# Kernel tuning notes

Hardware: AMD Instinct MI355X
Metric: run time of the kernel (lower is better)

Reference implementation:

```python
import jax, jax.numpy as jnp
import numpy as np

B, L, M = 4, 16384, 256
HID, FDIM, INNER, ODIM = 512, 128, 128, 3
HEADS, DH = 2, 64
NFREQ = 16  # feature_dim // (2 * input_dim)
ALPHA = 10.0
SIGMA_Q = 128.0
SIGMA_LS = (128.0, 32.0, 8.0)


def setup_inputs() -> dict:
    key = jax.random.key(0)
    ks = jax.random.split(key, 16)
    s = 0.02
    nl = len(SIGMA_LS)
    return {
        "x": jax.random.uniform(ks[0], (B, L, 4), jnp.float32),
        "tokens": jax.random.normal(ks[1], (B, M, HID), jnp.float32),
        "w_query": jax.random.normal(ks[2], (FDIM, HID), jnp.float32) * s,
        "b_query": jnp.zeros((HID,), jnp.float32),
        "w_to_q": jax.random.normal(ks[3], (HID, INNER), jnp.float32) * s,
        "w_to_kv": jax.random.normal(ks[4], (HID, 2 * INNER), jnp.float32) * s,
        "w_to_out": jax.random.normal(ks[5], (INNER, HID), jnp.float32) * s,
        "b_to_out": jnp.zeros((HID,), jnp.float32),
        "w_band": jax.random.normal(ks[6], (nl, FDIM, HID), jnp.float32) * s,
        "b_band": jnp.zeros((nl, HID), jnp.float32),
        "w_mod": jax.random.normal(ks[7], (nl, HID, HID), jnp.float32) * s,
        "b_mod": jnp.zeros((nl, HID), jnp.float32),
        "w_hv": jax.random.normal(ks[8], (nl - 1, HID, HID), jnp.float32) * s,
        "b_hv": jnp.zeros((nl - 1, HID), jnp.float32),
        "w_out": jax.random.normal(ks[9], (nl, HID, ODIM), jnp.float32) * s,
        "b_out": jnp.zeros((nl, ODIM), jnp.float32),
        "Dd": 8, "Hh": 16, "Ww": 16, "Tt": 8,
    }


def _calc_gamma(grid, omegas):
    # grid: [L, 4]; omegas: [NFREQ] -> gamma: [L, 4*2*NFREQ] = [L, FDIM]
    arg = jnp.pi * grid[:, :, None] * omegas[None, None, :]
    return jnp.concatenate([jnp.sin(arg), jnp.cos(arg)], axis=-1).reshape(grid.shape[0], -1)


def reference(x, tokens, w_query, b_query, w_to_q, w_to_kv, w_to_out, b_to_out,
              w_band, b_band, w_mod, b_mod, w_hv, b_hv, w_out, b_out, Dd, Hh, Ww, Tt):
    Bn, Ln, _ = x.shape
    m = tokens.shape[1]
    grid = x[0]  # grid shared across batch, exactly as in the torch module (uses x[0])

    # relative-position bias (ALiBi-like) from approximate patch indices
    z_i = (grid[:, 0] * Dd).astype(jnp.int32)
    y_i = (grid[:, 1] * Hh).astype(jnp.int32)
    x_i = (grid[:, 2] * Ww).astype(jnp.int32)
    t_i = (grid[:, 3] * Tt).astype(jnp.int32)
    idx = ((t_i * Dd + z_i) * Hh + y_i) * Ww + x_i  # [L]
    n_tot = Dd * Hh * Ww * Tt
    t = idx.astype(jnp.float32) / n_tot
    tok_pos = (jnp.arange(m, dtype=jnp.float32) + 0.5) / m
    bias = -ALPHA * (t[:, None] - tok_pos[None, :]) ** 2  # [L, m]

    # Fourier-feature query path (shared across batch)
    omegas_q = jnp.logspace(1.0, np.log10(SIGMA_Q), NFREQ, dtype=jnp.float32)
    x_q = jax.nn.relu(_calc_gamma(grid, omegas_q) @ w_query + b_query)  # [L, HID]

    # cross attention with additive bias
    q = (x_q @ w_to_q).reshape(Ln, HEADS, DH).transpose(1, 0, 2)  # [H, L, Dh]
    kv = tokens @ w_to_kv  # [B, m, 2*INNER]
    k, v = jnp.split(kv, 2, axis=-1)
    k = k.reshape(Bn, m, HEADS, DH).transpose(0, 2, 1, 3)  # [B, H, m, Dh]
    v = v.reshape(Bn, m, HEADS, DH).transpose(0, 2, 1, 3)
    sim = jnp.einsum('hld,bhmd->bhlm', q, k) * (DH ** -0.5) + bias[None, None]
    attn = jax.nn.softmax(sim, axis=-1)
    out = jnp.einsum('bhlm,bhmd->bhld', attn, v)
    out = out.transpose(0, 2, 1, 3).reshape(Bn, Ln, HEADS * DH)
    modv = out @ w_to_out + b_to_out  # [B, L, HID]

    # modulated MLP chain with residual hv accumulation
    total = jnp.zeros((Bn, Ln, w_out.shape[-1]), dtype=x.dtype)
    hv = None
    for kk in range(len(SIGMA_LS)):
        omg = jnp.logspace(1.0, np.log10(SIGMA_LS[kk]), NFREQ, dtype=jnp.float32)
        h_l = jax.nn.relu(_calc_gamma(grid, omg) @ w_band[kk] + b_band[kk])  # [L, HID]
        m_l = jax.nn.relu(h_l[None] + modv @ w_mod[kk] + b_mod[kk])  # [B, L, HID]
        if kk == 0:
            hv = m_l
        else:
            hv = jax.nn.relu((m_l + hv) @ w_hv[kk - 1] + b_hv[kk - 1])
        total = total + hv @ w_out[kk] + b_out[kk]
    return total  # [B, L, ODIM]
```

## Files before the change

### kernel.cpp

```cpp
#include <hip/hip_runtime.h>

#define L_N   16384
#define B_N   4
#define M_N   256
#define HID_N 512
#define PI_F  3.14159265358979323846f

typedef short short8 __attribute__((ext_vector_type(8)));
typedef float f32x4 __attribute__((ext_vector_type(4)));

__device__ __forceinline__ ushort f2bf(float f) {
  uint u = __float_as_uint(f);
  uint r = u + 0x7FFF + ((u >> 16) & 1);
  return (ushort)(r >> 16);
}
__device__ __forceinline__ float bf2f(ushort s) {
  return __uint_as_float(((uint)s) << 16);
}
__device__ __forceinline__ void gld_lds16(const void* g, void* s) {
  __builtin_amdgcn_global_load_lds((const __attribute__((address_space(1))) void*)g,
                                   (__attribute__((address_space(3))) void*)s, 16, 0, 0);
}

__global__ __launch_bounds__(256) void k_wt_all(
    const float* __restrict__ w_query, const float* __restrict__ w_to_q,
    const float* __restrict__ w_to_kv, const float* __restrict__ w_to_out,
    const float* __restrict__ w_band, const float* __restrict__ w_mod,
    const float* __restrict__ w_hv,
    ushort* __restrict__ wq_t, ushort* __restrict__ wtq_t,
    ushort* __restrict__ wkv_t, ushort* __restrict__ wto_t,
    ushort* __restrict__ wb_t, ushort* __restrict__ wm_t, ushort* __restrict__ whv_t) {
  __shared__ float t[32][33];
  int tb = blockIdx.x;
  const float* in; ushort* out; int R, C;
  if (tb < 64)        { in = w_query;  out = wq_t;  R = 128; C = 512; }
  else if (tb < 128)  { tb -= 64;  in = w_to_q;   out = wtq_t; R = 512; C = 128; }
  else if (tb < 256)  { tb -= 128; in = w_to_kv;  out = wkv_t; R = 512; C = 256; }
  else if (tb < 320)  { tb -= 256; in = w_to_out; out = wto_t; R = 128; C = 512; }
  else if (tb < 512)  { tb -= 320; int kk = tb >> 6; tb &= 63;
                        in = w_band + (size_t)kk * 65536; out = wb_t + (size_t)kk * 65536; R = 128; C = 512; }
  else if (tb < 1280) { tb -= 512; int kk = tb >> 8; tb &= 255;
                        in = w_mod + (size_t)kk * 262144; out = wm_t + (size_t)kk * 262144; R = 512; C = 512; }
  else                { tb -= 1280; int kk = tb >> 8; tb &= 255;
                        in = w_hv + (size_t)kk * 262144; out = whv_t + (size_t)kk * 262144; R = 512; C = 512; }
  int nbx = C >> 5;
  int bx = (tb % nbx) * 32, by = (tb / nbx) * 32;
  int tx = threadIdx.x & 31, ty = threadIdx.x >> 5;
#pragma unroll
  for (int j = 0; j < 32; j += 8) t[ty + j][tx] = in[(size_t)(by + ty + j) * C + bx + tx];
  __syncthreads();
#pragma unroll
  for (int j = 0; j < 32; j += 8)
    out[(size_t)(bx + ty + j) * R + by + tx] = f2bf(t[tx][ty + j]);
}

__global__ __launch_bounds__(256) void k_cvt(const float* __restrict__ in,
                                             ushort* __restrict__ out, int n4) {
  int i = blockIdx.x * 256 + threadIdx.x;
  if (i >= n4) return;
  float4 v = *(const float4*)&in[(size_t)i * 4];
  ushort* o = &out[(size_t)i * 4];
  o[0] = f2bf(v.x); o[1] = f2bf(v.y); o[2] = f2bf(v.z); o[3] = f2bf(v.w);
}

__global__ __launch_bounds__(256) void k_gamma(const float* __restrict__ x,
                                               ushort* __restrict__ gout) {
  __shared__ float om[16];
  const float lgs[4] = {2.1072099696478683f, 2.1072099696478683f,
                        1.5051499783199058f, 0.9030899869919435f};
  int spec = blockIdx.y;
  float lg = lgs[spec];
  int tid = threadIdx.x;
  if (tid < 16) om[tid] = powf(10.0f, 1.0f + (float)tid * ((lg - 1.0f) * (1.0f / 15.0f)));
  __syncthreads();
  int l0 = blockIdx.x * 16;
  int idx0 = tid * 8;
  int row = idx0 >> 7, f0 = idx0 & 127;
  int c = f0 >> 5;
  float g = x[(size_t)(l0 + row) * 4 + c];
  float base = PI_F * g;
  int w0 = f0 & 31;
  bool is_cos = (w0 >= 16);
  short8 o;
#pragma unroll
  for (int j = 0; j < 8; ++j) {
    int jf = (w0 + j) & 15;
    float arg = base * om[jf];
    float v = is_cos ? __cosf(arg) : __sinf(arg);
    o[j] = (short)f2bf(v);
  }
  *(short8*)&gout[(size_t)spec * L_N * 128 + (size_t)(l0 + row) * 128 + f0] = o;
}

__global__ __launch_bounds__(256) void k_tpos(const float* __restrict__ x,
                                              const int* dD, const int* dH,
                                              const int* dW, const int* dT,
                                              float* __restrict__ tbuf) {
  int l = blockIdx.x * 256 + threadIdx.x;
  float g0 = x[(size_t)l * 4 + 0], g1 = x[(size_t)l * 4 + 1];
  float g2 = x[(size_t)l * 4 + 2], g3 = x[(size_t)l * 4 + 3];
  int Dd = dD[0], Hh = dH[0], Ww = dW[0], Tt = dT[0];
  int zi = (int)(g0 * (float)Dd), yi = (int)(g1 * (float)Hh);
  int xi = (int)(g2 * (float)Ww), ti = (int)(g3 * (float)Tt);
  int idx = ((ti * Dd + zi) * Hh + yi) * Ww + xi;
  tbuf[l] = (float)idx / (float)(Dd * Hh * Ww * Tt);
}

__global__ __launch_bounds__(256, 4) void k_gemm2(
    const ushort* __restrict__ A, long long sA,
    const ushort* __restrict__ Wt,
    const float* __restrict__ bias,
    const ushort* __restrict__ add1,
    const ushort* add2, long long sAdd2,
    ushort* C, long long sC,
    const float* __restrict__ wout,
    float* __restrict__ opb,
    int zoff,
    int N, int K, int do_relu,
    int nbx, int nby, int nz) {
  __shared__ __align__(16) ushort S[128 * 64 * 2];
  __shared__ float woutL[384];
  ushort* As = S;
  ushort* Ws = S + 128 * 64;
  int tid = threadIdx.x;
  int lane = tid & 63, wid = tid >> 6;

  int nwg = nbx * nby * nz;
  int gid0 = blockIdx.x;
  int q = nwg >> 3, r = nwg & 7;
  int xcd = gid0 & 7, rank = gid0 >> 3;
  int sid = (xcd < r) ? (xcd * (q + 1) + rank) : (r * (q + 1) + (xcd - r) * q + rank);
  int z = sid / (nbx * nby);
  int rem = sid - z * (nbx * nby);
  int n0 = (rem % nbx) * 128, r0 = (rem / nbx) * 128;

  A += (size_t)z * sA;
  C += (size_t)z * sC;
  const ushort* a2p = add2 ? add2 + (size_t)z * sAdd2 : nullptr;
  int wr = wid >> 1, wc = wid & 1;
  int ksm = K >> 6;

  f32x4 acc[4][4];
#pragma unroll
  for (int i = 0; i < 4; ++i)
#pragma unroll
    for (int j = 0; j < 4; ++j) acc[i][j] = (f32x4)0.0f;

  for (int t = 0; t < ksm; ++t) {
#pragma unroll
    for (int j = 0; j < 4; ++j) {
      int sig = j * 256 + wid * 64 + lane;
      int rr = sig >> 3, ph = sig & 7, sl = ph ^ (rr & 7);
      gld_lds16(&A[(size_t)(r0 + rr) * K + t * 64 + sl * 8], &As[(size_t)(j * 256 + wid * 64) * 8]);
      gld_lds16(&Wt[(size_t)(n0 + rr) * K + t * 64 + sl * 8], &Ws[(size_t)(j * 256 + wid * 64) * 8]);
    }
    __syncthreads();
#pragma unroll
    for (int ks = 0; ks < 2; ++ks) {
      short8 af[4], bg[4];
#pragma unroll
      for (int fm = 0; fm < 4; ++fm) {
        int row = wr * 64 + fm * 16 + (lane & 15);
        af[fm] = *(const short8*)&As[row * 64 + (((ks * 4 + (lane >> 4)) ^ (row & 7)) * 8)];
      }
#pragma unroll
      for (int fn = 0; fn < 4; ++fn) {
        int nl = wc * 64 + fn * 16 + (lane & 15);
        bg[fn] = *(const short8*)&Ws[nl * 64 + (((ks * 4 + (lane >> 4)) ^ (nl & 7)) * 8)];
      }
#pragma unroll
      for (int fm = 0; fm < 4; ++fm)
#pragma unroll
        for (int fn = 0; fn < 4; ++fn)
          acc[fm][fn] = __builtin_amdgcn_mfma_f32_16x16x32_bf16(af[fm], bg[fn], acc[fm][fn], 0, 0, 0);
    }
    __syncthreads();
  }

  if (wout && tid < 128) {
    woutL[tid * 3 + 0] = wout[(size_t)(n0 + tid) * 3 + 0];
    woutL[tid * 3 + 1] = wout[(size_t)(n0 + tid) * 3 + 1];
    woutL[tid * 3 + 2] = wout[(size_t)(n0 + tid) * 3 + 2];
  }

  float* Ls = (float*)S;
  int row = tid >> 3;
  int c0 = (tid & 7) * 16;
#pragma unroll
  for (int fm = 0; fm < 4; ++fm) {
    if (fm) __syncthreads();
#pragma unroll
    for (int fn = 0; fn < 4; ++fn)
#pragma unroll
      for (int reg = 0; reg < 4; ++reg) {
        int lr = wr * 16 + (lane >> 4) * 4 + reg;
        int lc = wc * 64 + fn * 16 + (lane & 15);
        Ls[lr * 132 + lc] = acc[fm][fn][reg];
      }
    __syncthreads();
    int gr = r0 + (row >> 4) * 64 + fm * 16 + (row & 15);
    float so0 = 0.0f, so1 = 0.0f, so2 = 0.0f;
#pragma unroll
    for (int hh = 0; hh < 2; ++hh) {
      int cc = c0 + hh * 8;
      float v[8];
#pragma unroll
      for (int j = 0; j < 8; ++j) v[j] = Ls[row * 132 + cc + j];
      if (bias) {
#pragma unroll
        for (int j = 0; j < 8; ++j) v[j] += bias[n0 + cc + j];
      }
      if (add1) {
        short8 a1 = *(const short8*)&add1[(size_t)gr * N + n0 + cc];
#pragma unroll
        for (int j = 0; j < 8; ++j) v[j] += bf2f((ushort)a1[j]);
      }
      if (do_relu) {
#pragma unroll
        for (int j = 0; j < 8; ++j) v[j] = fmaxf(v[j], 0.0f);
      }
      if (a2p) {
        short8 a2 = *(const short8*)&a2p[(size_t)gr * N + n0 + cc];
#pragma unroll
        for (int j = 0; j < 8; ++j) v[j] += bf2f((ushort)a2[j]);
      }
      if (wout) {
#pragma unroll
        for (int j = 0; j < 8; ++j) {
          so0 = fmaf(v[j], woutL[(cc + j) * 3 + 0], so0);
          so1 = fmaf(v[j], woutL[(cc + j) * 3 + 1], so1);
          so2 = fmaf(v[j], woutL[(cc + j) * 3 + 2], so2);
        }
      }
      short8 ov;
#pragma unroll
      for (int j = 0; j < 8; ++j) ov[j] = (short)f2bf(v[j]);
      *(short8*)&C[(size_t)gr * N + n0 + cc] = ov;
    }
    if (wout) {
      so0 += __shfl_down(so0, 4); so1 += __shfl_down(so1, 4); so2 += __shfl_down(so2, 4);
      so0 += __shfl_down(so0, 2); so1 += __shfl_down(so1, 2); so2 += __shfl_down(so2, 2);
      so0 += __shfl_down(so0, 1); so1 += __shfl_down(so1, 1); so2 += __shfl_down(so2, 1);
      if ((tid & 7) == 0) {
        int bx = n0 >> 7;
        size_t oi = (((size_t)bx * 4 + (zoff + z)) * L_N + gr) * 3;
        opb[oi + 0] = so0; opb[oi + 1] = so1; opb[oi + 2] = so2;
      }
    }
  }
}

__global__ __launch_bounds__(256) void k_outred(const float* __restrict__ opb,
                                                const float* __restrict__ b_out,
                                                float* __restrict__ out) {
  int i = blockIdx.x * 256 + threadIdx.x;
  if (i >= B_N * L_N) return;
  float a0 = b_out[0] + b_out[3] + b_out[6];
  float a1 = b_out[1] + b_out[4] + b_out[7];
  float a2 = b_out[2] + b_out[5] + b_out[8];
  const size_t SS = (size_t)4 * B_N * L_N * 3;
#pragma unroll
  for (int slot = 0; slot < 3; ++slot)
#pragma unroll
    for (int bx = 0; bx < 4; ++bx) {
      const float* p = opb + slot * SS + (((size_t)bx * B_N * L_N) + i) * 3;
      a0 += p[0]; a1 += p[1]; a2 += p[2];
    }
  out[(size_t)i * 3 + 0] = a0;
  out[(size_t)i * 3 + 1] = a1;
  out[(size_t)i * 3 + 2] = a2;
}

__global__ __launch_bounds__(256) void k_rearr(const ushort* __restrict__ kvtmp,
                                               ushort* __restrict__ kbuf,
                                               ushort* __restrict__ vtb) {
  int i = blockIdx.x * 256 + threadIdx.x;
  int col = i & 255, row = i >> 8;
  int b = row >> 8, m = row & 255;
  ushort v = kvtmp[i];
  if (col < 128)
    kbuf[((size_t)b * 256 + m) * 128 + col] = v;
  else
    vtb[(size_t)b * 128 * 256 + (size_t)(col - 128) * 256 + m] = v;
}

__global__ __launch_bounds__(256) void k_attn_m(const ushort* __restrict__ qbuf,
                                                const float* __restrict__ tbuf,
                                                const ushort* __restrict__ kbuf,
                                                const ushort* __restrict__ vtb,
                                                ushort* __restrict__ attn) {
  __shared__ __align__(16) ushort Kt[256 * 64];
  __shared__ __align__(16) ushort Vt[64 * 256];
  __shared__ __align__(16) ushort Qs[64 * 64];
  __shared__ __align__(16) ushort Pw[4][16 * 40];
  __shared__ float ts[64];
  int tid = threadIdx.x;
  int lane = tid & 63, wid = tid >> 6;
  int l0 = blockIdx.x * 64;
  int h = blockIdx.y;
  int z = blockIdx.z;
  const ushort* kbuf_b = kbuf + (size_t)z * M_N * 128;
  const ushort* vtb_b = vtb + (size_t)z * 128 * M_N;
  ushort* attn_b = attn + (size_t)z * L_N * 128;
#pragma unroll
  for (int j = 0; j < 8; ++j) {
    int sig = j * 256 + wid * 64 + lane;
    int m = sig >> 3, ph = sig & 7, sl = ph ^ (m & 7);
    gld_lds16(&kbuf_b[(size_t)m * 128 + h * 64 + sl * 8], &Kt[(size_t)(j * 256 + wid * 64) * 8]);
  }
#pragma unroll
  for (int j = 0; j < 8; ++j) {
    int sig = j * 256 + wid * 64 + lane;
    int d = sig >> 5, ph = sig & 31, sl = ph ^ ((d & 7) << 2);
    gld_lds16(&vtb_b[(size_t)(h * 64 + d) * 256 + sl * 8], &Vt[(size_t)(j * 256 + wid * 64) * 8]);
  }
#pragma unroll
  for (int j = 0; j < 2; ++j) {
    int sig = j * 256 + wid * 64 + lane;
    int q = sig >> 3, ph = sig & 7, sl = ph ^ (q & 7);
    gld_lds16(&qbuf[(size_t)(l0 + q) * 128 + h * 64 + sl * 8], &Qs[(size_t)(j * 256 + wid * 64) * 8]);
  }
  if (tid < 64) ts[tid] = tbuf[l0 + tid];
  __syncthreads();

  f32x4 s_acc[16];
#pragma unroll
  for (int fn = 0; fn < 16; ++fn) s_acc[fn] = (f32x4)0.0f;
#pragma unroll
  for (int ks = 0; ks < 2; ++ks) {
    int qrow = wid * 16 + (lane & 15);
    short8 aq = *(const short8*)&Qs[qrow * 64 + (((ks * 4 + (lane >> 4)) ^ (qrow & 7)) * 8)];
#pragma unroll
    for (int fn = 0; fn < 16; ++fn) {
      int m = fn * 16 + (lane & 15);
      short8 bk = *(const short8*)&Kt[m * 64 + (((ks * 4 + (lane >> 4)) ^ (m & 7)) * 8)];
      s_acc[fn] = __builtin_amdgcn_mfma_f32_16x16x32_bf16(aq, bk, s_acc[fn], 0, 0, 0);
    }
  }
  float mx[4] = {-1e30f, -1e30f, -1e30f, -1e30f};
#pragma unroll
  for (int fn = 0; fn < 16; ++fn) {
#pragma unroll
    for (int reg = 0; reg < 4; ++reg) {
      int ql = wid * 16 + (lane >> 4) * 4 + reg;
      int m = fn * 16 + (lane & 15);
      float mp = ((float)m + 0.5f) * (1.0f / 256.0f);
      float d = ts[ql] - mp;
      float v = s_acc[fn][reg] * 0.125f - 10.0f * d * d;
      s_acc[fn][reg] = v;
      mx[reg] = fmaxf(mx[reg], v);
    }
  }
#pragma unroll
  for (int reg = 0; reg < 4; ++reg) {
    mx[reg] = fmaxf(mx[reg], __shfl_xor(mx[reg], 1));
    mx[reg] = fmaxf(mx[reg], __shfl_xor(mx[reg], 2));
    mx[reg] = fmaxf(mx[reg], __shfl_xor(mx[reg], 4));
    mx[reg] = fmaxf(mx[reg], __shfl_xor(mx[reg], 8));
  }
  float sm[4] = {0.0f, 0.0f, 0.0f, 0.0f};
#pragma unroll
  for (int fn = 0; fn < 16; ++fn) {
#pragma unroll
    for (int reg = 0; reg < 4; ++reg) {
      float e = __expf(s_acc[fn][reg] - mx[reg]);
      s_acc[fn][reg] = e;
      sm[reg] += e;
    }
  }
#pragma unroll
  for (int reg = 0; reg < 4; ++reg) {
    sm[reg] += __shfl_xor(sm[reg], 1);
    sm[reg] += __shfl_xor(sm[reg], 2);
    sm[reg] += __shfl_xor(sm[reg], 4);
    sm[reg] += __shfl_xor(sm[reg], 8);
  }
  float inv[4];
#pragma unroll
  for (int reg = 0; reg < 4; ++reg) inv[reg] = 1.0f / sm[reg];

  f32x4 o_acc[4];
#pragma unroll
  for (int fn = 0; fn < 4; ++fn) o_acc[fn] = (f32x4)0.0f;
  for (int kk = 0; kk < 8; ++kk) {
#pragma unroll
    for (int fp = 0; fp < 2; ++fp) {
      int fn = kk * 2 + fp;
#pragma unroll
      for (int reg = 0; reg < 4; ++reg) {
        int ql16 = (lane >> 4) * 4 + reg;
        int mc = fp * 16 + (lane & 15);
        Pw[wid][ql16 * 40 + mc] = f2bf(s_acc[fn][reg] * inv[reg]);
      }
    }
    asm volatile("s_waitcnt lgkmcnt(0)" ::: "memory");
    __builtin_amdgcn_sched_barrier(0);
    short8 pa = *(const short8*)&Pw[wid][(lane & 15) * 40 + (lane >> 4) * 8];
#pragma unroll
    for (int fn = 0; fn < 4; ++fn) {
      int dr = fn * 16 + (lane & 15);
      short8 vb = *(const short8*)&Vt[dr * 256 + (((kk * 4 + (lane >> 4)) ^ ((dr & 7) << 2)) * 8)];
      o_acc[fn] = __builtin_amdgcn_mfma_f32_16x16x32_bf16(pa, vb, o_acc[fn], 0, 0, 0);
    }
    asm volatile("s_waitcnt lgkmcnt(0)" ::: "memory");
    __builtin_amdgcn_sched_barrier(0);
  }
#pragma unroll
  for (int fn = 0; fn < 4; ++fn)
#pragma unroll
    for (int reg = 0; reg < 4; ++reg) {
      int ql = l0 + wid * 16 + (lane >> 4) * 4 + reg;
      attn_b[(size_t)ql * 128 + h * 64 + fn * 16 + (lane & 15)] = f2bf(o_acc[fn][reg]);
    }
}

extern "C" void kernel_launch(void* const* d_in, const int* in_sizes, int n_in,
                              void* d_out, int out_size, void* d_ws, size_t ws_size,
                              hipStream_t stream) {
  const float* x        = (const float*)d_in[0];
  const float* tokens   = (const float*)d_in[1];
  const float* w_query  = (const float*)d_in[2];
  const float* b_query  = (const float*)d_in[3];
  const float* w_to_q   = (const float*)d_in[4];
  const float* w_to_kv  = (const float*)d_in[5];
  const float* w_to_out = (const float*)d_in[6];
  const float* b_to_out = (const float*)d_in[7];
  const float* w_band   = (const float*)d_in[8];
  const float* b_band   = (const float*)d_in[9];
  const float* w_mod    = (const float*)d_in[10];
  const float* b_mod    = (const float*)d_in[11];
  const float* w_hv     = (const float*)d_in[12];
  const float* b_hv     = (const float*)d_in[13];
  const float* w_out    = (const float*)d_in[14];
  const float* b_out    = (const float*)d_in[15];
  const int* Dd = (const int*)d_in[16];
  const int* Hh = (const int*)d_in[17];
  const int* Ww = (const int*)d_in[18];
  const int* Tt = (const int*)d_in[19];
  float* out = (float*)d_out;

  ushort* W = (ushort*)d_ws;
  size_t o = 0;
  auto alloc = [&](size_t n) { ushort* p = W + o; o += n; return p; };
  const size_t big = (size_t)L_N * HID_N;
  const size_t LQ = (size_t)L_N * 128;
  const size_t OPB_U = (size_t)3 * 4 * B_N * L_N * 3 * 2;

  ushort* gamma  = alloc(4 * LQ);
  ushort* qb     = alloc(LQ);
  ushort* attnout= alloc(4 * LQ);
  ushort* tokb   = alloc((size_t)B_N * M_N * HID_N);
  ushort* kbuf   = alloc((size_t)B_N * M_N * 128);
  ushort* vtb    = alloc((size_t)B_N * 128 * M_N);
  ushort* wq_t   = alloc(512 * 128);
  ushort* wtq_t  = alloc(128 * 512);
  ushort* wkv_t  = alloc(256 * 512);
  ushort* wto_t  = alloc(512 * 128);
  ushort* wb_t   = alloc(3 * 512 * 128);
  ushort* wm_t   = alloc(3 * 512 * 512);
  ushort* whv_t  = alloc(2 * 512 * 512);
  float* tbuf    = (float*)alloc(L_N * 2);
  size_t base_u = o;

  size_t need_batched = (base_u + big + 3 * 4 * big) * sizeof(ushort);
  bool batched = ws_size >= need_batched;

  ushort* hband; float* opb; ushort *modv, *hv, *tmp;
  if (batched) {
    hband = alloc(big);
    modv = alloc(4 * big); hv = alloc(4 * big); tmp = alloc(4 * big);
    opb = (float*)attnout;
  } else {
    hband = alloc(3 * big);
    opb = (float*)alloc(OPB_U);
    modv = alloc(big); hv = alloc(big); tmp = alloc(big);
  }
  ushort* xq = modv;
  ushort* kvtmp = attnout;

  const long long SL = (long long)big;
  const long long SQ = (long long)LQ;
  const size_t SLOT = (size_t)4 * B_N * L_N * 3;

  k_wt_all<<<dim3(1792), 256, 0, stream>>>(w_query, w_to_q, w_to_kv, w_to_out, w_band, w_mod, w_hv,
                                           wq_t, wtq_t, wkv_t, wto_t, wb_t, wm_t, whv_t);
  k_cvt<<<dim3(512), 256, 0, stream>>>(tokens, tokb, B_N * M_N * HID_N / 4);
  k_gamma<<<dim3(L_N / 16, 4), 256, 0, stream>>>(x, gamma);
  k_tpos<<<dim3(L_N / 256), 256, 0, stream>>>(x, Dd, Hh, Ww, Tt, tbuf);

  k_gemm2<<<dim3(4 * 128), 256, 0, stream>>>(gamma, 0, wq_t, b_query, nullptr, nullptr, 0,
                                             xq, 0, nullptr, nullptr, 0, 512, 128, 1, 4, 128, 1);
  k_gemm2<<<dim3(1 * 128), 256, 0, stream>>>(xq, 0, wtq_t, nullptr, nullptr, nullptr, 0,
                                             qb, 0, nullptr, nullptr, 0, 128, 512, 0, 1, 128, 1);
  k_gemm2<<<dim3(2 * 8), 256, 0, stream>>>(tokb, 0, wkv_t, nullptr, nullptr, nullptr, 0,
                                           kvtmp, 0, nullptr, nullptr, 0, 256, 512, 0, 2, 8, 1);
  k_rearr<<<dim3(1024), 256, 0, stream>>>(kvtmp, kbuf, vtb);
  k_attn_m<<<dim3(L_N / 64, 2, 4), 256, 0, stream>>>(qb, tbuf, kbuf, vtb, attnout);

  if (batched) {
    k_gemm2<<<dim3(4 * 128 * 4), 256, 0, stream>>>(attnout, SQ, wto_t, b_to_out, nullptr, nullptr, 0,
                                                   modv, SL, nullptr, nullptr, 0, 512, 128, 0, 4, 128, 4);
    for (int kk = 0; kk < 3; ++kk) {
      k_gemm2<<<dim3(4 * 128), 256, 0, stream>>>(gamma + (size_t)(1 + kk) * LQ, 0,
                                                 wb_t + (size_t)kk * 65536, b_band + kk * 512,
                                                 nullptr, nullptr, 0, hband, 0,
                                                 nullptr, nullptr, 0, 512, 128, 1, 4, 128, 1);
      if (kk == 0) {
        k_gemm2<<<dim3(4 * 128 * 4), 256, 0, stream>>>(modv, SL, wm_t, b_mod, hband, nullptr, 0,
                                                       hv, SL, w_out, opb, 0, 512, 512, 1, 4, 128, 4);
      } else {
        k_gemm2<<<dim3(4 * 128 * 4), 256, 0, stream>>>(modv, SL, wm_t + (size_t)kk * 262144,
                                                       b_mod + kk * 512, hband, hv, SL,
                                                       tmp, SL, nullptr, nullptr, 0, 512, 512, 1, 4, 128, 4);
        k_gemm2<<<dim3(4 * 128 * 4), 256, 0, stream>>>(tmp, SL, whv_t + (size_t)(kk - 1) * 262144,
                                                       b_hv + (kk - 1) * 512, nullptr, nullptr, 0,
                                                       hv, SL, w_out + (size_t)kk * 1536,
                                                       opb + (size_t)kk * SLOT, 0, 512, 512, 1, 4, 128, 4);
      }
    }
  } else {
    for (int kk = 0; kk < 3; ++kk)
      k_gemm2<<<dim3(4 * 128), 256, 0, stream>>>(gamma + (size_t)(1 + kk) * LQ, 0,
                                                 wb_t + (size_t)kk * 65536, b_band + kk * 512,
                                                 nullptr, nullptr, 0, hband + (size_t)kk * big, 0,
                                                 nullptr, nullptr, 0, 512, 128, 1, 4, 128, 1);
    for (int z = 0; z < B_N; ++z) {
      k_gemm2<<<dim3(4 * 128), 256, 0, stream>>>(attnout + (size_t)z * LQ, 0, wto_t, b_to_out,
                                                 nullptr, nullptr, 0, modv, 0,
                                                 nullptr, nullptr, 0, 512, 128, 0, 4, 128, 1);
      k_gemm2<<<dim3(4 * 128), 256, 0, stream>>>(modv, 0, wm_t, b_mod, hband, nullptr, 0,
                                                 hv, 0, w_out, opb, z, 512, 512, 1, 4, 128, 1);
      for (int kk = 1; kk < 3; ++kk) {
        k_gemm2<<<dim3(4 * 128), 256, 0, stream>>>(modv, 0, wm_t + (size_t)kk * 262144,
                                                   b_mod + kk * 512, hband + (size_t)kk * big, hv, 0,
                                                   tmp, 0, nullptr, nullptr, 0, 512, 512, 1, 4, 128, 1);
        k_gemm2<<<dim3(4 * 128), 256, 0, stream>>>(tmp, 0, whv_t + (size_t)(kk - 1) * 262144,
                                                   b_hv + (kk - 1) * 512, nullptr, nullptr, 0,
                                                   hv, 0, w_out + (size_t)kk * 1536,
                                                   opb + (size_t)kk * SLOT, z, 512, 512, 1, 4, 128, 1);
      }
    }
  }
  k_outred<<<dim3((B_N * L_N + 255) / 256), 256, 0, stream>>>(opb, b_out, out);
}
```

Before: 437.9 us.

## Fuse three modulation GEMMs into one wide GEMM and add residual at A-load

The three w_mod GEMMs per batch chunk are merged into a single N=1536 launch that writes segmented outputs (each with its own band add and relu). The hv residual add moves from the GEMM epilogue into the next GEMM's A-tile load, which now reads two bf16 inputs and sums them into LDS through registers instead of async global-to-LDS loads. The three band GEMMs become one batched launch, and batches are processed in chunks of 1 or 2 depending on workspace. This cuts kernel launches and the tmp write/read round trip, at the cost of a slower register-path A load and a smaller batch grouping than the old batched path.

Result: slower. 470.4 us (+7.4%).

```diff
diff --git a/kernel.cpp b/kernel.cpp
--- a/kernel.cpp
+++ b/kernel.cpp
@@ -108,15 +108,13 @@
 
 __global__ __launch_bounds__(256, 4) void k_gemm2(
     const ushort* __restrict__ A, long long sA,
-    const ushort* __restrict__ Wt,
-    const float* __restrict__ bias,
-    const ushort* __restrict__ add1,
-    const ushort* add2, long long sAdd2,
-    ushort* C, long long sC,
-    const float* __restrict__ wout,
-    float* __restrict__ opb,
-    int zoff,
-    int N, int K, int do_relu,
+    const ushort* __restrict__ A2, long long sA2,
+    const ushort* __restrict__ Wt, long long sWt,
+    const float* __restrict__ bias, int sBias,
+    const ushort* __restrict__ add1, long long sA1seg,
+    ushort* C, long long sC, long long sSeg,
+    const float* __restrict__ wout, float* __restrict__ opb, int zoff,
+    int segMode, int N, int K, int do_relu,
     int nbx, int nby, int nz) {
   __shared__ __align__(16) ushort S[128 * 64 * 2];
   __shared__ float woutL[384];
@@ -135,8 +133,17 @@
   int n0 = (rem % nbx) * 128, r0 = (rem / nbx) * 128;
 
   A += (size_t)z * sA;
-  C += (size_t)z * sC;
-  const ushort* a2p = add2 ? add2 + (size_t)z * sAdd2 : nullptr;
+  const ushort* A2p = A2 ? A2 + (size_t)z * sA2 : nullptr;
+  const ushort* Wtp = Wt + (size_t)z * sWt;
+  const float* biasp = bias ? bias + (size_t)z * sBias : nullptr;
+
+  int seg = segMode ? (n0 >> 9) : 0;
+  int ncol0 = segMode ? (n0 & 511) : n0;
+  int rowN = segMode ? 512 : N;
+  ushort* Cp = C ? C + (size_t)seg * sSeg + (size_t)z * sC : nullptr;
+  const ushort* a1p = add1 ? add1 + (size_t)seg * sA1seg : nullptr;
+  const float* woutEff = (wout && n0 < 512) ? wout : nullptr;
+
   int wr = wid >> 1, wc = wid & 1;
   int ksm = K >> 6;
 
@@ -147,12 +154,29 @@
     for (int j = 0; j < 4; ++j) acc[i][j] = (f32x4)0.0f;
 
   for (int t = 0; t < ksm; ++t) {
-#pragma unroll
-    for (int j = 0; j < 4; ++j) {
-      int sig = j * 256 + wid * 64 + lane;
-      int rr = sig >> 3, ph = sig & 7, sl = ph ^ (rr & 7);
-      gld_lds16(&A[(size_t)(r0 + rr) * K + t * 64 + sl * 8], &As[(size_t)(j * 256 + wid * 64) * 8]);
-      gld_lds16(&Wt[(size_t)(n0 + rr) * K + t * 64 + sl * 8], &Ws[(size_t)(j * 256 + wid * 64) * 8]);
+    if (A2p) {
+#pragma unroll
+      for (int j = 0; j < 4; ++j) {
+        int sig = j * 256 + tid;
+        int rr = sig >> 3, ph = sig & 7, sl = ph ^ (rr & 7);
+        size_t go = (size_t)(r0 + rr) * K + t * 64 + sl * 8;
+        short8 va = *(const short8*)&A[go];
+        short8 vb = *(const short8*)&A2p[go];
+        short8 vs;
+#pragma unroll
+        for (int e = 0; e < 8; ++e)
+          vs[e] = (short)f2bf(bf2f((ushort)va[e]) + bf2f((ushort)vb[e]));
+        *(short8*)&As[(size_t)sig * 8] = vs;
+        gld_lds16(&Wtp[(size_t)(n0 + rr) * K + t * 64 + sl * 8], &Ws[(size_t)sig * 8]);
+      }
+    } else {
+#pragma unroll
+      for (int j = 0; j < 4; ++j) {
+        int sig = j * 256 + tid;
+        int rr = sig >> 3, ph = sig & 7, sl = ph ^ (rr & 7);
+        gld_lds16(&A[(size_t)(r0 + rr) * K + t * 64 + sl * 8], &As[(size_t)sig * 8]);
+        gld_lds16(&Wtp[(size_t)(n0 + rr) * K + t * 64 + sl * 8], &Ws[(size_t)sig * 8]);
+      }
     }
     __syncthreads();
 #pragma unroll
@@ -177,10 +201,10 @@
     __syncthreads();
   }
 
-  if (wout && tid < 128) {
-    woutL[tid * 3 + 0] = wout[(size_t)(n0 + tid) * 3 + 0];
-    woutL[tid * 3 + 1] = wout[(size_t)(n0 + tid) * 3 + 1];
-    woutL[tid * 3 + 2] = wout[(size_t)(n0 + tid) * 3 + 2];
+  if (woutEff && tid < 128) {
+    woutL[tid * 3 + 0] = woutEff[(size_t)(n0 + tid) * 3 + 0];
+    woutL[tid * 3 + 1] = woutEff[(size_t)(n0 + tid) * 3 + 1];
+    woutL[tid * 3 + 2] = woutEff[(size_t)(n0 + tid) * 3 + 2];
   }
 
   float* Ls = (float*)S;
@@ -206,12 +230,12 @@
       float v[8];
 #pragma unroll
       for (int j = 0; j < 8; ++j) v[j] = Ls[row * 132 + cc + j];
-      if (bias) {
-#pragma unroll
-        for (int j = 0; j < 8; ++j) v[j] += bias[n0 + cc + j];
-      }
-      if (add1) {
-        short8 a1 = *(const short8*)&add1[(size_t)gr * N + n0 + cc];
+      if (biasp) {
+#pragma unroll
+        for (int j = 0; j < 8; ++j) v[j] += biasp[n0 + cc + j];
+      }
+      if (a1p) {
+        short8 a1 = *(const short8*)&a1p[(size_t)gr * 512 + ncol0 + cc];
 #pragma unroll
         for (int j = 0; j < 8; ++j) v[j] += bf2f((ushort)a1[j]);
       }
@@ -219,12 +243,7 @@
 #pragma unroll
         for (int j = 0; j < 8; ++j) v[j] = fmaxf(v[j], 0.0f);
       }
-      if (a2p) {
-        short8 a2 = *(const short8*)&a2p[(size_t)gr * N + n0 + cc];
-#pragma unroll
-        for (int j = 0; j < 8; ++j) v[j] += bf2f((ushort)a2[j]);
-      }
-      if (wout) {
+      if (woutEff) {
 #pragma unroll
         for (int j = 0; j < 8; ++j) {
           so0 = fmaf(v[j], woutL[(cc + j) * 3 + 0], so0);
@@ -232,12 +251,14 @@
           so2 = fmaf(v[j], woutL[(cc + j) * 3 + 2], so2);
         }
       }
-      short8 ov;
-#pragma unroll
-      for (int j = 0; j < 8; ++j) ov[j] = (short)f2bf(v[j]);
-      *(short8*)&C[(size_t)gr * N + n0 + cc] = ov;
-    }
-    if (wout) {
+      if (Cp) {
+        short8 ov;
+#pragma unroll
+        for (int j = 0; j < 8; ++j) ov[j] = (short)f2bf(v[j]);
+        *(short8*)&Cp[(size_t)gr * rowN + ncol0 + cc] = ov;
+      }
+    }
+    if (woutEff) {
       so0 += __shfl_down(so0, 4); so1 += __shfl_down(so1, 4); so2 += __shfl_down(so2, 4);
       so0 += __shfl_down(so0, 2); so1 += __shfl_down(so1, 2); so2 += __shfl_down(so2, 2);
       so0 += __shfl_down(so0, 1); so1 += __shfl_down(so1, 1); so2 += __shfl_down(so2, 1);
@@ -444,7 +465,6 @@
   auto alloc = [&](size_t n) { ushort* p = W + o; o += n; return p; };
   const size_t big = (size_t)L_N * HID_N;
   const size_t LQ = (size_t)L_N * 128;
-  const size_t OPB_U = (size_t)3 * 4 * B_N * L_N * 3 * 2;
 
   ushort* gamma  = alloc(4 * LQ);
   ushort* qb     = alloc(LQ);
@@ -462,25 +482,18 @@
   float* tbuf    = (float*)alloc(L_N * 2);
   size_t base_u = o;
 
-  size_t need_batched = (base_u + big + 3 * 4 * big) * sizeof(ushort);
-  bool batched = ws_size >= need_batched;
-
-  ushort* hband; float* opb; ushort *modv, *hv, *tmp;
-  if (batched) {
-    hband = alloc(big);
-    modv = alloc(4 * big); hv = alloc(4 * big); tmp = alloc(4 * big);
-    opb = (float*)attnout;
-  } else {
-    hband = alloc(3 * big);
-    opb = (float*)alloc(OPB_U);
-    modv = alloc(big); hv = alloc(big); tmp = alloc(big);
-  }
+  int NZ = (ws_size >= (base_u + 13 * big) * sizeof(ushort)) ? 2 : 1;
+  ushort* modv  = alloc((size_t)NZ * big);
+  ushort* hband = alloc(3 * big);
+  ushort* m_all = alloc(3 * (size_t)NZ * big);
+  ushort* hv1   = alloc((size_t)NZ * big);
   ushort* xq = modv;
   ushort* kvtmp = attnout;
-
-  const long long SL = (long long)big;
-  const long long SQ = (long long)LQ;
+  float* opb = (float*)gamma;
   const size_t SLOT = (size_t)4 * B_N * L_N * 3;
+
+  const long long BG = (long long)big;
+  const long long LQs = (long long)LQ;
 
   k_wt_all<<<dim3(1792), 256, 0, stream>>>(w_query, w_to_q, w_to_kv, w_to_out, w_band, w_mod, w_hv,
                                            wq_t, wtq_t, wkv_t, wto_t, wb_t, wm_t, whv_t);
@@ -488,58 +501,39 @@
   k_gamma<<<dim3(L_N / 16, 4), 256, 0, stream>>>(x, gamma);
   k_tpos<<<dim3(L_N / 256), 256, 0, stream>>>(x, Dd, Hh, Ww, Tt, tbuf);
 
-  k_gemm2<<<dim3(4 * 128), 256, 0, stream>>>(gamma, 0, wq_t, b_query, nullptr, nullptr, 0,
-                                             xq, 0, nullptr, nullptr, 0, 512, 128, 1, 4, 128, 1);
-  k_gemm2<<<dim3(1 * 128), 256, 0, stream>>>(xq, 0, wtq_t, nullptr, nullptr, nullptr, 0,
-                                             qb, 0, nullptr, nullptr, 0, 128, 512, 0, 1, 128, 1);
-  k_gemm2<<<dim3(2 * 8), 256, 0, stream>>>(tokb, 0, wkv_t, nullptr, nullptr, nullptr, 0,
-                                           kvtmp, 0, nullptr, nullptr, 0, 256, 512, 0, 2, 8, 1);
+  k_gemm2<<<dim3(4 * 128), 256, 0, stream>>>(gamma, 0, nullptr, 0, wq_t, 0, b_query, 0,
+                                             nullptr, 0, xq, 0, 0, nullptr, nullptr, 0,
+                                             0, 512, 128, 1, 4, 128, 1);
+  k_gemm2<<<dim3(1 * 128), 256, 0, stream>>>(xq, 0, nullptr, 0, wtq_t, 0, nullptr, 0,
+                                             nullptr, 0, qb, 0, 0, nullptr, nullptr, 0,
+                                             0, 128, 512, 0, 1, 128, 1);
+  k_gemm2<<<dim3(2 * 8), 256, 0, stream>>>(tokb, 0, nullptr, 0, wkv_t, 0, nullptr, 0,
+                                           nullptr, 0, kvtmp, 0, 0, nullptr, nullptr, 0,
+                                           0, 256, 512, 0, 2, 8, 1);
   k_rearr<<<dim3(1024), 256, 0, stream>>>(kvtmp, kbuf, vtb);
   k_attn_m<<<dim3(L_N / 64, 2, 4), 256, 0, stream>>>(qb, tbuf, kbuf, vtb, attnout);
-
-  if (batched) {
-    k_gemm2<<<dim3(4 * 128 * 4), 256, 0, stream>>>(attnout, SQ, wto_t, b_to_out, nullptr, nullptr, 0,
-                                                   modv, SL, nullptr, nullptr, 0, 512, 128, 0, 4, 128, 4);
-    for (int kk = 0; kk < 3; ++kk) {
-      k_gemm2<<<dim3(4 * 128), 256, 0, stream>>>(gamma + (size_t)(1 + kk) * LQ, 0,
-                                                 wb_t + (size_t)kk * 65536, b_band + kk * 512,
-                                                 nullptr, nullptr, 0, hband, 0,
-                                                 nullptr, nullptr, 0, 512, 128, 1, 4, 128, 1);
-      if (kk == 0) {
-        k_gemm2<<<dim3(4 * 128 * 4), 256, 0, stream>>>(modv, SL, wm_t, b_mod, hband, nullptr, 0,
-                                                       hv, SL, w_out, opb, 0, 512, 512, 1, 4, 128, 4);
-      } else {
-        k_gemm2<<<dim3(4 * 128 * 4), 256, 0, stream>>>(modv, SL, wm_t + (size_t)kk * 262144,
-                                                       b_mod + kk * 512, hband, hv, SL,
-                                                       tmp, SL, nullptr, nullptr, 0, 512, 512, 1, 4, 128, 4);
-        k_gemm2<<<dim3(4 * 128 * 4), 256, 0, stream>>>(tmp, SL, whv_t + (size_t)(kk - 1) * 262144,
-                                                       b_hv + (kk - 1) * 512, nullptr, nullptr, 0,
-                                                       hv, SL, w_out + (size_t)kk * 1536,
-                                                       opb + (size_t)kk * SLOT, 0, 512, 512, 1, 4, 128, 4);
-      }
-    }
-  } else {
-    for (int kk = 0; kk < 3; ++kk)
-      k_gemm2<<<dim3(4 * 128), 256, 0, stream>>>(gamma + (size_t)(1 + kk) * LQ, 0,
-                                                 wb_t + (size_t)kk * 65536, b_band + kk * 512,
-                                                 nullptr, nullptr, 0, hband + (size_t)kk * big, 0,
-                                                 nullptr, nullptr, 0, 512, 128, 1, 4, 128, 1);
-    for (int z = 0; z < B_N; ++z) {
-      k_gemm2<<<dim3(4 * 128), 256, 0, stream>>>(attnout + (size_t)z * LQ, 0, wto_t, b_to_out,
-                                                 nullptr, nullptr, 0, modv, 0,
-                                                 nullptr, nullptr, 0, 512, 128, 0, 4, 128, 1);
-      k_gemm2<<<dim3(4 * 128), 256, 0, stream>>>(modv, 0, wm_t, b_mod, hband, nullptr, 0,
-                                                 hv, 0, w_out, opb, z, 512, 512, 1, 4, 128, 1);
-      for (int kk = 1; kk < 3; ++kk) {
-        k_gemm2<<<dim3(4 * 128), 256, 0, stream>>>(modv, 0, wm_t + (size_t)kk * 262144,
-                                                   b_mod + kk * 512, hband + (size_t)kk * big, hv, 0,
-                                                   tmp, 0, nullptr, nullptr, 0, 512, 512, 1, 4, 128, 1);
-        k_gemm2<<<dim3(4 * 128), 256, 0, stream>>>(tmp, 0, whv_t + (size_t)(kk - 1) * 262144,
-                                                   b_hv + (kk - 1) * 512, nullptr, nullptr, 0,
-                                                   hv, 0, w_out + (size_t)kk * 1536,
-                                                   opb + (size_t)kk * SLOT, z, 512, 512, 1, 4, 128, 1);
-      }
-    }
+  k_gemm2<<<dim3(4 * 128 * 3), 256, 0, stream>>>(gamma + LQ, LQs, nullptr, 0, wb_t, 65536,
+                                                 b_band, 512, nullptr, 0, hband, BG, 0,
+                                                 nullptr, nullptr, 0, 0, 512, 128, 1, 4, 128, 3);
+
+  for (int zoff = 0; zoff < B_N; zoff += NZ) {
+    k_gemm2<<<dim3(4 * 128 * NZ), 256, 0, stream>>>(attnout + (size_t)zoff * LQ, LQs, nullptr, 0,
+                                                    wto_t, 0, b_to_out, 0, nullptr, 0,
+                                                    modv, BG, 0, nullptr, nullptr, 0,
+                                                    0, 512, 128, 0, 4, 128, NZ);
+    k_gemm2<<<dim3(12 * 128 * NZ), 256, 0, stream>>>(modv, BG, nullptr, 0, wm_t, 0,
+                                                     b_mod, 0, hband, BG,
+                                                     m_all, BG, (long long)NZ * big,
+                                                     w_out, opb, zoff,
+                                                     1, 1536, 512, 1, 12, 128, NZ);
+    k_gemm2<<<dim3(4 * 128 * NZ), 256, 0, stream>>>(m_all + (size_t)NZ * big, BG, m_all, BG,
+                                                    whv_t, 0, b_hv, 0, nullptr, 0,
+                                                    hv1, BG, 0, w_out + 1536, opb + SLOT, zoff,
+                                                    0, 512, 512, 1, 4, 128, NZ);
+    k_gemm2<<<dim3(4 * 128 * NZ), 256, 0, stream>>>(m_all + (size_t)2 * NZ * big, BG, hv1, BG,
+                                                    whv_t + 262144, 0, b_hv + 512, 0, nullptr, 0,
+                                                    nullptr, 0, 0, w_out + 2 * 1536, opb + 2 * SLOT, zoff,
+                                                    0, 512, 512, 1, 4, 128, NZ);
   }
   k_outred<<<dim3((B_N * L_N + 255) / 256), 256, 0, stream>>>(opb, b_out, out);
 }
```

## Batch band GEMMs across levels and chunk batch dimension to fit workspace

Applied to the files above, without the earlier changes.

Adds per-z weight and bias strides to the GEMM kernel so the three band-projection GEMMs run in one launch over all levels. The batch dimension is then processed in chunks of two (or one) instead of all four at once, with the opb partials stored in the gamma buffer. This trades the fully batched path for a smaller workspace footprint and a better-cached working set, at the cost of more launches and smaller grids per launch.

Result: slower. 448.6 us (+2.4%).

```diff
diff --git a/kernel.cpp b/kernel.cpp
--- a/kernel.cpp
+++ b/kernel.cpp
@@ -108,8 +108,8 @@
 
 __global__ __launch_bounds__(256, 4) void k_gemm2(
     const ushort* __restrict__ A, long long sA,
-    const ushort* __restrict__ Wt,
-    const float* __restrict__ bias,
+    const ushort* __restrict__ Wt, long long sWt,
+    const float* __restrict__ bias, int sBias,
     const ushort* __restrict__ add1,
     const ushort* add2, long long sAdd2,
     ushort* C, long long sC,
@@ -136,6 +136,8 @@
 
   A += (size_t)z * sA;
   C += (size_t)z * sC;
+  const ushort* Wtp = Wt + (size_t)z * sWt;
+  const float* biasp = bias ? bias + (size_t)z * sBias : nullptr;
   const ushort* a2p = add2 ? add2 + (size_t)z * sAdd2 : nullptr;
   int wr = wid >> 1, wc = wid & 1;
   int ksm = K >> 6;
@@ -152,7 +154,7 @@
       int sig = j * 256 + wid * 64 + lane;
       int rr = sig >> 3, ph = sig & 7, sl = ph ^ (rr & 7);
       gld_lds16(&A[(size_t)(r0 + rr) * K + t * 64 + sl * 8], &As[(size_t)(j * 256 + wid * 64) * 8]);
-      gld_lds16(&Wt[(size_t)(n0 + rr) * K + t * 64 + sl * 8], &Ws[(size_t)(j * 256 + wid * 64) * 8]);
+      gld_lds16(&Wtp[(size_t)(n0 + rr) * K + t * 64 + sl * 8], &Ws[(size_t)(j * 256 + wid * 64) * 8]);
     }
     __syncthreads();
 #pragma unroll
@@ -206,9 +208,9 @@
       float v[8];
 #pragma unroll
       for (int j = 0; j < 8; ++j) v[j] = Ls[row * 132 + cc + j];
-      if (bias) {
-#pragma unroll
-        for (int j = 0; j < 8; ++j) v[j] += bias[n0 + cc + j];
+      if (biasp) {
+#pragma unroll
+        for (int j = 0; j < 8; ++j) v[j] += biasp[n0 + cc + j];
       }
       if (add1) {
         short8 a1 = *(const short8*)&add1[(size_t)gr * N + n0 + cc];
@@ -444,7 +446,6 @@
   auto alloc = [&](size_t n) { ushort* p = W + o; o += n; return p; };
   const size_t big = (size_t)L_N * HID_N;
   const size_t LQ = (size_t)L_N * 128;
-  const size_t OPB_U = (size_t)3 * 4 * B_N * L_N * 3 * 2;
 
   ushort* gamma  = alloc(4 * LQ);
   ushort* qb     = alloc(LQ);
@@ -462,24 +463,17 @@
   float* tbuf    = (float*)alloc(L_N * 2);
   size_t base_u = o;
 
-  size_t need_batched = (base_u + big + 3 * 4 * big) * sizeof(ushort);
-  bool batched = ws_size >= need_batched;
-
-  ushort* hband; float* opb; ushort *modv, *hv, *tmp;
-  if (batched) {
-    hband = alloc(big);
-    modv = alloc(4 * big); hv = alloc(4 * big); tmp = alloc(4 * big);
-    opb = (float*)attnout;
-  } else {
-    hband = alloc(3 * big);
-    opb = (float*)alloc(OPB_U);
-    modv = alloc(big); hv = alloc(big); tmp = alloc(big);
-  }
+  int NZ = (ws_size >= (base_u + 9 * big) * sizeof(ushort)) ? 2 : 1;
+  ushort* hband = alloc(3 * big);
+  ushort* modv  = alloc((size_t)NZ * big);
+  ushort* hv    = alloc((size_t)NZ * big);
+  ushort* tmp   = alloc((size_t)NZ * big);
   ushort* xq = modv;
   ushort* kvtmp = attnout;
-
-  const long long SL = (long long)big;
-  const long long SQ = (long long)LQ;
+  float* opb = (float*)gamma;
+
+  const long long BG = (long long)big;
+  const long long LQs = (long long)LQ;
   const size_t SLOT = (size_t)4 * B_N * L_N * 3;
 
   k_wt_all<<<dim3(1792), 256, 0, stream>>>(w_query, w_to_q, w_to_kv, w_to_out, w_band, w_mod, w_hv,
@@ -488,56 +482,38 @@
   k_gamma<<<dim3(L_N / 16, 4), 256, 0, stream>>>(x, gamma);
   k_tpos<<<dim3(L_N / 256), 256, 0, stream>>>(x, Dd, Hh, Ww, Tt, tbuf);
 
-  k_gemm2<<<dim3(4 * 128), 256, 0, stream>>>(gamma, 0, wq_t, b_query, nullptr, nullptr, 0,
+  k_gemm2<<<dim3(4 * 128), 256, 0, stream>>>(gamma, 0, wq_t, 0, b_query, 0, nullptr, nullptr, 0,
                                              xq, 0, nullptr, nullptr, 0, 512, 128, 1, 4, 128, 1);
-  k_gemm2<<<dim3(1 * 128), 256, 0, stream>>>(xq, 0, wtq_t, nullptr, nullptr, nullptr, 0,
+  k_gemm2<<<dim3(1 * 128), 256, 0, stream>>>(xq, 0, wtq_t, 0, nullptr, 0, nullptr, nullptr, 0,
                                              qb, 0, nullptr, nullptr, 0, 128, 512, 0, 1, 128, 1);
-  k_gemm2<<<dim3(2 * 8), 256, 0, stream>>>(tokb, 0, wkv_t, nullptr, nullptr, nullptr, 0,
+  k_gemm2<<<dim3(2 * 8), 256, 0, stream>>>(tokb, 0, wkv_t, 0, nullptr, 0, nullptr, nullptr, 0,
                                            kvtmp, 0, nullptr, nullptr, 0, 256, 512, 0, 2, 8, 1);
   k_rearr<<<dim3(1024), 256, 0, stream>>>(kvtmp, kbuf, vtb);
   k_attn_m<<<dim3(L_N / 64, 2, 4), 256, 0, stream>>>(qb, tbuf, kbuf, vtb, attnout);
-
-  if (batched) {
-    k_gemm2<<<dim3(4 * 128 * 4), 256, 0, stream>>>(attnout, SQ, wto_t, b_to_out, nullptr, nullptr, 0,
-                                                   modv, SL, nullptr, nullptr, 0, 512, 128, 0, 4, 128, 4);
+  k_gemm2<<<dim3(4 * 128 * 3), 256, 0, stream>>>(gamma + LQ, LQs, wb_t, 65536, b_band, 512,
+                                                 nullptr, nullptr, 0, hband, BG,
+                                                 nullptr, nullptr, 0, 512, 128, 1, 4, 128, 3);
+
+  for (int zoff = 0; zoff < B_N; zoff += NZ) {
+    k_gemm2<<<dim3(4 * 128 * NZ), 256, 0, stream>>>(attnout + (size_t)zoff * LQ, LQs, wto_t, 0,
+                                                    b_to_out, 0, nullptr, nullptr, 0,
+                                                    modv, BG, nullptr, nullptr, 0,
+                                                    512, 128, 0, 4, 128, NZ);
     for (int kk = 0; kk < 3; ++kk) {
-      k_gemm2<<<dim3(4 * 128), 256, 0, stream>>>(gamma + (size_t)(1 + kk) * LQ, 0,
-                                                 wb_t + (size_t)kk * 65536, b_band + kk * 512,
-                                                 nullptr, nullptr, 0, hband, 0,
-                                                 nullptr, nullptr, 0, 512, 128, 1, 4, 128, 1);
       if (kk == 0) {
-        k_gemm2<<<dim3(4 * 128 * 4), 256, 0, stream>>>(modv, SL, wm_t, b_mod, hband, nullptr, 0,
-                                                       hv, SL, w_out, opb, 0, 512, 512, 1, 4, 128, 4);
+        k_gemm2<<<dim3(4 * 128 * NZ), 256, 0, stream>>>(modv, BG, wm_t, 0, b_mod, 0, hband,
+                                                        nullptr, 0, hv, BG,
+                                                        w_out, opb, zoff, 512, 512, 1, 4, 128, NZ);
       } else {
-        k_gemm2<<<dim3(4 * 128 * 4), 256, 0, stream>>>(modv, SL, wm_t + (size_t)kk * 262144,
-                                                       b_mod + kk * 512, hband, hv, SL,
-                                                       tmp, SL, nullptr, nullptr, 0, 512, 512, 1, 4, 128, 4);
-        k_gemm2<<<dim3(4 * 128 * 4), 256, 0, stream>>>(tmp, SL, whv_t + (size_t)(kk - 1) * 262144,
-                                                       b_hv + (kk - 1) * 512, nullptr, nullptr, 0,
-                                                       hv, SL, w_out + (size_t)kk * 1536,
-                                                       opb + (size_t)kk * SLOT, 0, 512, 512, 1, 4, 128, 4);
-      }
-    }
-  } else {
-    for (int kk = 0; kk < 3; ++kk)
-      k_gemm2<<<dim3(4 * 128), 256, 0, stream>>>(gamma + (size_t)(1 + kk) * LQ, 0,
-                                                 wb_t + (size_t)kk * 65536, b_band + kk * 512,
-                                                 nullptr, nullptr, 0, hband + (size_t)kk * big, 0,
-                                                 nullptr, nullptr, 0, 512, 128, 1, 4, 128, 1);
-    for (int z = 0; z < B_N; ++z) {
-      k_gemm2<<<dim3(4 * 128), 256, 0, stream>>>(attnout + (size_t)z * LQ, 0, wto_t, b_to_out,
-                                                 nullptr, nullptr, 0, modv, 0,
-                                                 nullptr, nullptr, 0, 512, 128, 0, 4, 128, 1);
-      k_gemm2<<<dim3(4 * 128), 256, 0, stream>>>(modv, 0, wm_t, b_mod, hband, nullptr, 0,
-                                                 hv, 0, w_out, opb, z, 512, 512, 1, 4, 128, 1);
-      for (int kk = 1; kk < 3; ++kk) {
-        k_gemm2<<<dim3(4 * 128), 256, 0, stream>>>(modv, 0, wm_t + (size_t)kk * 262144,
-                                                   b_mod + kk * 512, hband + (size_t)kk * big, hv, 0,
-                                                   tmp, 0, nullptr, nullptr, 0, 512, 512, 1, 4, 128, 1);
-        k_gemm2<<<dim3(4 * 128), 256, 0, stream>>>(tmp, 0, whv_t + (size_t)(kk - 1) * 262144,
-                                                   b_hv + (kk - 1) * 512, nullptr, nullptr, 0,
-                                                   hv, 0, w_out + (size_t)kk * 1536,
-                                                   opb + (size_t)kk * SLOT, z, 512, 512, 1, 4, 128, 1);
+        k_gemm2<<<dim3(4 * 128 * NZ), 256, 0, stream>>>(modv, BG, wm_t + (size_t)kk * 262144, 0,
+                                                        b_mod + kk * 512, 0, hband + (size_t)kk * big,
+                                                        hv, BG, tmp, BG,
+                                                        nullptr, nullptr, 0, 512, 512, 1, 4, 128, NZ);
+        k_gemm2<<<dim3(4 * 128 * NZ), 256, 0, stream>>>(tmp, BG, whv_t + (size_t)(kk - 1) * 262144, 0,
+                                                        b_hv + (kk - 1) * 512, 0, nullptr,
+                                                        nullptr, 0, hv, BG,
+                                                        w_out + (size_t)kk * 1536, opb + (size_t)kk * SLOT,
+                                                        zoff, 512, 512, 1, 4, 128, NZ);
       }
     }
   }
```
